# Performance work log

Hardware: AMD Instinct MI355X
Metric: run time of the kernel (lower is better)

## Reference

```python
import jax, jax.numpy as jnp
import numpy as np

NT, NV, ND, NM, NP = 50000, 1000, 20000, 5000, 8000
E = 100000
D, H, C = 256, 4, 64          # gnn_hidden_dim, heads, per-head channels
TS_FEAT, EMB, L = 64, 128, 2
NEG_SLOPE = 0.2

SIZES = {'ts': NT, 'vital': NV, 'diag': ND, 'med': NM, 'proc': NP}
EDGE_TYPES = [('ts', 'vital'), ('vital', 'ts'), ('ts', 'diag'), ('diag', 'ts'),
              ('ts', 'med'), ('med', 'ts'), ('ts', 'proc'), ('proc', 'ts')]
T = len(EDGE_TYPES)


def setup_inputs():
    key = jax.random.key(0)
    ks = jax.random.split(key, 32)
    def nrm(k, shape, s=0.05):
        return jax.random.normal(k, shape, dtype=jnp.float32) * s
    inp = {}
    inp['ts_x'] = nrm(ks[0], (NT, TS_FEAT), 1.0)
    inp['emb_vital'] = nrm(ks[1], (NV, EMB), 1.0)
    inp['emb_diag'] = nrm(ks[2], (ND, EMB), 1.0)
    inp['emb_med'] = nrm(ks[3], (NM, EMB), 1.0)
    inp['emb_proc'] = nrm(ks[4], (NP, EMB), 1.0)
    inp['Wp_ts'] = nrm(ks[5], (TS_FEAT, D)); inp['bp_ts'] = jnp.zeros((D,), jnp.float32)
    inp['Wp_c'] = nrm(ks[6], (4, EMB, D)); inp['bp_c'] = jnp.zeros((4, D), jnp.float32)
    inp['Wsrc'] = nrm(ks[7], (L, T, D, H * C))
    inp['Wdst'] = nrm(ks[8], (L, T, D, H * C))
    inp['asrc'] = nrm(ks[9], (L, T, H, C))
    inp['adst'] = nrm(ks[10], (L, T, H, C))
    inp['bconv'] = jnp.zeros((L, T, H * C), jnp.float32)
    inp['Wc1'] = nrm(ks[11], (D, D // 2)); inp['bc1'] = jnp.zeros((D // 2,), jnp.float32)
    inp['Wc2'] = nrm(ks[12], (D // 2, 1)); inp['bc2'] = jnp.zeros((1,), jnp.float32)
    names = ['ei_tv', 'ei_vt', 'ei_td', 'ei_dt', 'ei_tm', 'ei_mt', 'ei_tp', 'ei_pt']
    for i, ((s, d), nm) in enumerate(zip(EDGE_TYPES, names)):
        k1, k2 = jax.random.split(ks[13 + i])
        src = jax.random.randint(k1, (E,), 0, SIZES[s], dtype=jnp.int32)
        dst = jax.random.randint(k2, (E,), 0, SIZES[d], dtype=jnp.int32)
        inp[nm] = jnp.stack([src, dst])
    return inp


def gat_conv(xs, xd, Ws, Wd, a_s, a_d, b, ei, nd):
    """Bipartite PyG GATConv: add_self_loops=False, concat heads, eval (no dropout)."""
    hs = (xs @ Ws).reshape(-1, H, C)            # [Ns,H,C]
    hd = (xd @ Wd).reshape(-1, H, C)            # [Nd,H,C]
    es = jnp.sum(hs * a_s, axis=-1)             # [Ns,H]
    ed = jnp.sum(hd * a_d, axis=-1)             # [Nd,H]
    src, dst = ei[0], ei[1]
    e = jax.nn.leaky_relu(es[src] + ed[dst], NEG_SLOPE)   # [E,H]
    m = jax.ops.segment_max(e, dst, num_segments=nd)      # segment softmax over dst
    ex = jnp.exp(e - m[dst])
    den = jax.ops.segment_sum(ex, dst, num_segments=nd)
    alpha = ex / (den[dst] + 1e-16)
    msg = (alpha[:, :, None] * hs[src]).reshape(-1, H * C)  # [E,H*C]
    return jax.ops.segment_sum(msg, dst, num_segments=nd) + b


def _forward(ts_x, emb_vital, emb_diag, emb_med, emb_proc, Wp_ts, bp_ts, Wp_c, bp_c,
             Wsrc, Wdst, asrc, adst, bconv, Wc1, bc1, Wc2, bc2, edges):
    x = {'ts': ts_x @ Wp_ts + bp_ts,
         'vital': emb_vital @ Wp_c[0] + bp_c[0],
         'diag': emb_diag @ Wp_c[1] + bp_c[1],
         'med': emb_med @ Wp_c[2] + bp_c[2],
         'proc': emb_proc @ Wp_c[3] + bp_c[3]}
    for l in range(L):
        new = {k: jnp.zeros((SIZES[k], D), jnp.float32) for k in x}  # HeteroConv aggr='sum'
        for t, ((s, d), ei) in enumerate(zip(EDGE_TYPES, edges)):
            new[d] = new[d] + gat_conv(x[s], x[d], Wsrc[l, t], Wdst[l, t],
                                       asrc[l, t], adst[l, t], bconv[l, t], ei, SIZES[d])
        x = {k: jax.nn.relu(v) for k, v in new.items()}
    g = jnp.mean(x['ts'], axis=0)               # graph embedding
    h = jax.nn.relu(g @ Wc1 + bc1)
    logits = h @ Wc2 + bc2
    return jnp.squeeze(logits, -1)              # output_classes == 1 -> scalar


def reference(ts_x, emb_vital, emb_diag, emb_med, emb_proc, Wp_ts, bp_ts, Wp_c, bp_c,
              Wsrc, Wdst, asrc, adst, bconv, Wc1, bc1, Wc2, bc2,
              ei_tv, ei_vt, ei_td, ei_dt, ei_tm, ei_mt, ei_tp, ei_pt):
    edges = (ei_tv, ei_vt, ei_td, ei_dt, ei_tm, ei_mt, ei_tp, ei_pt)
    return _forward(ts_x, emb_vital, emb_diag, emb_med, emb_proc, Wp_ts, bp_ts, Wp_c, bp_c,
                    Wsrc, Wdst, asrc, adst, bconv, Wc1, bc1, Wc2, bc2, edges)
```

## Files before the change

kernel.cpp:

```cpp
#include <hip/hip_runtime.h>

#define E_N 100000
#define NTOT 84000
#define NDST 234000

typedef __attribute__((ext_vector_type(8))) short bfrag8;
typedef __attribute__((ext_vector_type(4))) float accf4;

__device__ __forceinline__ void atomAddF(float* p, float v) {
    unsafeAtomicAdd(p, v);
}

__device__ __forceinline__ float lrelu(float v) { return v >= 0.f ? v : 0.2f * v; }

__device__ __forceinline__ unsigned short f2bf(float f) {
    unsigned u = __float_as_uint(f);
    return (unsigned short)((u + 0x7FFFu + ((u >> 16) & 1u)) >> 16);
}
__device__ __forceinline__ float bf2f(unsigned short h) {
    return __uint_as_float(((unsigned)h) << 16);
}

__constant__ int c_tbase[8] = {0, 1000, 51000, 71000, 121000, 126000, 176000, 184000};

struct EI8 { const int* p[8]; };

struct BTJob { const float* W; unsigned short* hi; unsigned short* lo; int K; int kshift; };
struct BTBatch { BTJob j[17]; };

__global__ __launch_bounds__(256) void makeBT(BTBatch b)
{
    BTJob jb = b.j[blockIdx.z];
    int idx = blockIdx.x * 256 + threadIdx.x;
    if (idx >= (jb.K << 8)) return;
    int n = idx >> jb.kshift;
    int k = idx & (jb.K - 1);
    float w = jb.W[(size_t)k * 256 + n];
    unsigned short h = f2bf(w);
    jb.hi[idx] = h;
    jb.lo[idx] = f2bf(w - bf2f(h));
}

struct MJob { const float* A; const unsigned short* BThi; const unsigned short* BTlo;
              float* C; unsigned short* Cbf; const float* bias; int M; int K; int relu; };
struct MBatch { MJob j[8]; };

__global__ __launch_bounds__(256, 2) void gemm_mfma(MBatch batch)
{
    const MJob jb = batch.j[blockIdx.z];
    const int bx = blockIdx.x;
    const int rowblk = (bx >> 4) * 8 + (bx & 7);
    const int half = (bx >> 3) & 1;
    const int bm = rowblk * 128;
    if (bm >= jb.M) return;
    const int bn = half * 128;
    const int M = jb.M, K = jb.K;

    __shared__ unsigned short Ah[128 * 40];
    __shared__ unsigned short Al[128 * 40];
    __shared__ unsigned short B1[128 * 40];
    __shared__ unsigned short B2[128 * 40];

    const int tid  = threadIdx.x;
    const int wv   = tid >> 6;
    const int lane = tid & 63;
    const int qr = wv >> 1, qc = wv & 1;
    const int lm = lane & 15;
    const int lq = lane >> 4;

    accf4 acc[4][4] = {};

    for (int k0 = 0; k0 < K; k0 += 32) {
#pragma unroll
        for (int it = 0; it < 4; ++it) {
            int slot = it * 256 + tid;
            int m  = slot >> 3;
            int kq = (slot & 7) << 2;
            float4 v = make_float4(0.f, 0.f, 0.f, 0.f);
            if (bm + m < M) v = *(const float4*)(jb.A + (size_t)(bm + m) * K + k0 + kq);
            int o = m * 40 + kq;
            unsigned short h0 = f2bf(v.x), h1 = f2bf(v.y), h2 = f2bf(v.z), h3 = f2bf(v.w);
            Ah[o + 0] = h0; Ah[o + 1] = h1; Ah[o + 2] = h2; Ah[o + 3] = h3;
            Al[o + 0] = f2bf(v.x - bf2f(h0));
            Al[o + 1] = f2bf(v.y - bf2f(h1));
            Al[o + 2] = f2bf(v.z - bf2f(h2));
            Al[o + 3] = f2bf(v.w - bf2f(h3));
        }
#pragma unroll
        for (int it = 0; it < 2; ++it) {
            int slot = it * 256 + tid;
            int n  = slot >> 2;
            int kq = (slot & 3) << 3;
            size_t go = (size_t)(bn + n) * K + k0 + kq;
            *(uint4*)&B1[n * 40 + kq] = *(const uint4*)(jb.BThi + go);
            *(uint4*)&B2[n * 40 + kq] = *(const uint4*)(jb.BTlo + go);
        }
        __syncthreads();

        bfrag8 ah[4], al[4], b1[4], b2[4];
#pragma unroll
        for (int t = 0; t < 4; ++t) {
            int am  = qr * 64 + t * 16 + lm;
            int bnn = qc * 64 + t * 16 + lm;
            ah[t] = *(const bfrag8*)&Ah[am * 40 + lq * 8];
            al[t] = *(const bfrag8*)&Al[am * 40 + lq * 8];
            b1[t] = *(const bfrag8*)&B1[bnn * 40 + lq * 8];
            b2[t] = *(const bfrag8*)&B2[bnn * 40 + lq * 8];
        }
#pragma unroll
        for (int mt = 0; mt < 4; ++mt)
#pragma unroll
            for (int nt = 0; nt < 4; ++nt) {
                acc[mt][nt] = __builtin_amdgcn_mfma_f32_16x16x32_bf16(ah[mt], b1[nt], acc[mt][nt], 0, 0, 0);
                acc[mt][nt] = __builtin_amdgcn_mfma_f32_16x16x32_bf16(al[mt], b1[nt], acc[mt][nt], 0, 0, 0);
                acc[mt][nt] = __builtin_amdgcn_mfma_f32_16x16x32_bf16(ah[mt], b2[nt], acc[mt][nt], 0, 0, 0);
            }
        __syncthreads();
    }

#pragma unroll
    for (int nt = 0; nt < 4; ++nt) {
        int col = bn + qc * 64 + nt * 16 + lm;
        float bv = jb.bias ? jb.bias[col] : 0.f;
#pragma unroll
        for (int mt = 0; mt < 4; ++mt) {
            int row0 = bm + qr * 64 + mt * 16 + lq * 4;
#pragma unroll
            for (int r = 0; r < 4; ++r) {
                int row = row0 + r;
                if (row < M) {
                    float o = acc[mt][nt][r] + bv;
                    if (jb.relu) o = fmaxf(o, 0.f);
                    if (jb.C)   jb.C[(size_t)row * 256 + col] = o;
                    if (jb.Cbf) jb.Cbf[(size_t)row * 256 + col] = f2bf(o);
                }
            }
        }
    }
}

__global__ __launch_bounds__(256) void fill_weff(const float* __restrict__ Wsrc,
                                                 const float* __restrict__ Wdst,
                                                 const float* __restrict__ asrc,
                                                 const float* __restrict__ adst,
                                                 float* __restrict__ weff)
{
    int idx = blockIdx.x * 256 + threadIdx.x;
    if (idx >= 81920) return;
    int col = idx & 31;
    int k   = (idx >> 5) & 255;
    int lnt = idx >> 13;
    int nt  = lnt % 5;
    int l   = lnt / 5;
    bool is_src; int t, h;
    if (nt == 0) {
        if (col < 16) { is_src = true;  t = (col >> 2) * 2;            h = col & 3; }
        else          { is_src = false; t = ((col - 16) >> 2) * 2 + 1; h = col & 3; }
    } else {
        if (col < 4)      { is_src = true;  t = 2 * nt - 1; h = col; }
        else if (col < 8) { is_src = false; t = 2 * nt - 2; h = col - 4; }
        else { weff[idx] = 0.f; return; }
    }
    const float* W = (is_src ? Wsrc : Wdst) + ((size_t)((l * 8 + t) * 256 + k)) * 256 + h * 64;
    const float* a = (is_src ? asrc : adst) + ((size_t)((l * 8 + t) * 4 + h)) * 64;
    float val = 0.f;
    for (int c = 0; c < 64; c++) val += W[c] * a[c];
    weff[idx] = val;
}

__global__ __launch_bounds__(256) void fillEff(const float* __restrict__ Wp_ts,
                                               const float* __restrict__ bp_ts,
                                               const float* __restrict__ Wp_c,
                                               const float* __restrict__ bp_c,
                                               const float* __restrict__ weff,
                                               float* __restrict__ effT,
                                               float* __restrict__ biasT,
                                               float* __restrict__ effC,
                                               float* __restrict__ biasC)
{
    int idx = blockIdx.x * 256 + threadIdx.x;
    if (idx < 2048) {
        int kk = idx >> 5, j = idx & 31;
        float s = 0.f;
        for (int k = 0; k < 256; k++) s += Wp_ts[kk * 256 + k] * weff[k * 32 + j];
        effT[idx] = s;
    } else if (idx < 2080) {
        int j = idx - 2048;
        float s = 0.f;
        for (int k = 0; k < 256; k++) s += bp_ts[k] * weff[k * 32 + j];
        biasT[j] = s;
    } else if (idx < 2080 + 4 * 1032) {
        int r = idx - 2080;
        int q = r / 1032; r -= q * 1032;
        const float* wq = weff + (q + 1) * 8192;
        if (r < 1024) {
            int kk = r >> 3, j = r & 7;
            float s = 0.f;
            for (int k = 0; k < 256; k++) s += Wp_c[(size_t)q * 32768 + kk * 256 + k] * wq[k * 32 + j];
            effC[(q * 128 + kk) * 8 + j] = s;
        } else {
            int j = r - 1024;
            float s = 0.f;
            for (int k = 0; k < 256; k++) s += bp_c[q * 256 + k] * wq[k * 32 + j];
            biasC[q * 8 + j] = s;
        }
    }
}

__global__ __launch_bounds__(256) void attnprojA(const float* __restrict__ ts_x,
                                                 const float* __restrict__ effT,
                                                 const float* __restrict__ biasT,
                                                 float* __restrict__ attnT)
{
    int n = blockIdx.x * 256 + threadIdx.x;
    if (n >= 50000) return;
    float acc[32];
#pragma unroll
    for (int j = 0; j < 32; j++) acc[j] = biasT[j];
    const float* xr = ts_x + (size_t)n * 64;
    for (int k = 0; k < 64; k += 4) {
        float4 xv = *(const float4*)(xr + k);
#pragma unroll
        for (int j = 0; j < 32; j++)
            acc[j] += xv.x * effT[(k + 0) * 32 + j] + xv.y * effT[(k + 1) * 32 + j]
                    + xv.z * effT[(k + 2) * 32 + j] + xv.w * effT[(k + 3) * 32 + j];
    }
#pragma unroll
    for (int j = 0; j < 32; j++) attnT[(size_t)n * 32 + j] = acc[j];
}

__global__ __launch_bounds__(256) void attnprojC1(const float* __restrict__ e0,
                                                  const float* __restrict__ e1,
                                                  const float* __restrict__ e2,
                                                  const float* __restrict__ e3,
                                                  const float* __restrict__ effC,
                                                  const float* __restrict__ biasC,
                                                  float* __restrict__ attnC)
{
    int m = blockIdx.x * 256 + threadIdx.x;
    if (m >= 34000) return;
    int q, loc;
    if (m < 1000)       { q = 0; loc = m; }
    else if (m < 21000) { q = 1; loc = m - 1000; }
    else if (m < 26000) { q = 2; loc = m - 21000; }
    else                { q = 3; loc = m - 26000; }
    const float* er = (q == 0 ? e0 : q == 1 ? e1 : q == 2 ? e2 : e3) + (size_t)loc * 128;
    const float* W = effC + q * 1024;
    float acc[8];
#pragma unroll
    for (int j = 0; j < 8; j++) acc[j] = biasC[q * 8 + j];
    for (int k = 0; k < 128; k += 4) {
        float4 xv = *(const float4*)(er + k);
#pragma unroll
        for (int j = 0; j < 8; j++)
            acc[j] += xv.x * W[(k + 0) * 8 + j] + xv.y * W[(k + 1) * 8 + j]
                    + xv.z * W[(k + 2) * 8 + j] + xv.w * W[(k + 3) * 8 + j];
    }
#pragma unroll
    for (int j = 0; j < 8; j++) attnC[(size_t)m * 8 + j] = acc[j];
}

template<int NO>
__device__ __forceinline__ void attnproj_body(const float* __restrict__ xrow,
                                              const float* __restrict__ W,
                                              float* __restrict__ out)
{
    float acc[NO];
#pragma unroll
    for (int j = 0; j < NO; j++) acc[j] = 0.f;
    for (int k = 0; k < 256; k += 4) {
        const float4 xv = *(const float4*)(xrow + k);
#pragma unroll
        for (int j = 0; j < NO; j++) {
            acc[j] += xv.x * W[(k + 0) * 32 + j] + xv.y * W[(k + 1) * 32 + j]
                    + xv.z * W[(k + 2) * 32 + j] + xv.w * W[(k + 3) * 32 + j];
        }
    }
#pragma unroll
    for (int j = 0; j < NO; j++) out[j] = acc[j];
}

__global__ __launch_bounds__(256) void attnprojC2(const float* __restrict__ x1,
                                                  const float* __restrict__ weff_l,
                                                  float* __restrict__ attnC)
{
    int m = blockIdx.x * 256 + threadIdx.x;
    if (m >= 34000) return;
    int n = 50000 + m;
    int nt = (n < 51000) ? 1 : (n < 71000) ? 2 : (n < 76000) ? 3 : 4;
    attnproj_body<8>(x1 + (size_t)n * 256, weff_l + nt * 8192, attnC + (size_t)m * 8);
}

__global__ __launch_bounds__(256) void count_k(EI8 ei, int* __restrict__ cnt)
{
    int g = blockIdx.x * 256 + threadIdx.x;
    if (g >= 8 * E_N) return;
    int t = g / E_N;
    int i = g - t * E_N;
    int d = ei.p[t][E_N + i];
    atomicAdd(&cnt[c_tbase[t] + d], 1);
}

__global__ __launch_bounds__(256) void scanA(const int* __restrict__ cnt,
                                             int* __restrict__ rowptr,
                                             int* __restrict__ bsum)
{
    __shared__ int sd[256];
    int b = blockIdx.x, t = threadIdx.x;
    int base = b * 1024 + t * 4;
    int v0 = 0, v1 = 0, v2 = 0, v3 = 0;
    if (base + 0 < NDST) v0 = cnt[base + 0];
    if (base + 1 < NDST) v1 = cnt[base + 1];
    if (base + 2 < NDST) v2 = cnt[base + 2];
    if (base + 3 < NDST) v3 = cnt[base + 3];
    int s = v0 + v1 + v2 + v3;
    sd[t] = s;
    __syncthreads();
    for (int off = 1; off < 256; off <<= 1) {
        int x = 0;
        if (t >= off) x = sd[t - off];
        __syncthreads();
        if (t >= off) sd[t] += x;
        __syncthreads();
    }
    int run = sd[t] - s;
    if (t == 255) bsum[b] = sd[255];
    if (base + 0 < NDST) rowptr[base + 0] = run;          run += v0;
    if (base + 1 < NDST) rowptr[base + 1] = run;          run += v1;
    if (base + 2 < NDST) rowptr[base + 2] = run;          run += v2;
    if (base + 3 < NDST) rowptr[base + 3] = run;
}

__global__ __launch_bounds__(256) void scanB(int* __restrict__ bsum, int nb)
{
    __shared__ int sd[256];
    int t = threadIdx.x;
    int v = (t < nb) ? bsum[t] : 0;
    sd[t] = v;
    __syncthreads();
    for (int off = 1; off < 256; off <<= 1) {
        int x = 0;
        if (t >= off) x = sd[t - off];
        __syncthreads();
        if (t >= off) sd[t] += x;
        __syncthreads();
    }
    if (t < nb) bsum[t] = sd[t] - v;
}

__global__ __launch_bounds__(256) void scanC(int* __restrict__ rowptr,
                                             const int* __restrict__ bsum,
                                             int* __restrict__ cursor)
{
    int b = blockIdx.x, t = threadIdx.x;
    int off = bsum[b];
    int base = b * 1024 + t * 4;
#pragma unroll
    for (int j = 0; j < 4; j++) {
        int i = base + j;
        if (i < NDST) {
            int r = rowptr[i] + off;
            rowptr[i] = r;
            cursor[i] = r;
        }
    }
    if (b == 0 && t == 0) rowptr[NDST] = 8 * E_N;
}

__global__ __launch_bounds__(256) void place_k(EI8 ei, int* __restrict__ cursor,
                                               int* __restrict__ ssrc)
{
    int g = blockIdx.x * 256 + threadIdx.x;
    if (g >= 8 * E_N) return;
    int t = g / E_N;
    int i = g - t * E_N;
    int d = ei.p[t][E_N + i];
    int s = ei.p[t][i];
    int pos = atomicAdd(&cursor[c_tbase[t] + d], 1);
    ssrc[pos] = s;
}

__global__ __launch_bounds__(256) void aggx_k(const float* __restrict__ attnT,
                                              const float* __restrict__ attnC,
                                              const unsigned short* __restrict__ xtsbf,
                                              const int* __restrict__ rowptr,
                                              const int* __restrict__ ssrc,
                                              float* __restrict__ aggx)
{
    int w = blockIdx.x * 4 + (threadIdx.x >> 6);
    int lane = threadIdx.x & 63;
    int h = lane >> 4;
    int ch = (h << 6) | ((lane & 15) << 2);
    int q, dloc;
    if (w < 1000)       { q = 0; dloc = w; }
    else if (w < 21000) { q = 1; dloc = w - 1000; }
    else if (w < 26000) { q = 2; dloc = w - 21000; }
    else                { q = 3; dloc = w - 26000; }
    const int csr4[4]  = {0, 51000, 121000, 176000};
    const int soff4[4] = {0, 4, 8, 12};
    int soff = soff4[q];
    int r0 = rowptr[csr4[q] + dloc], r1 = rowptr[csr4[q] + dloc + 1];
    float ed = attnC[(size_t)w * 8 + 4 + h];
    float den = 0.f, sx = 0.f, sy = 0.f, sz = 0.f, sw = 0.f;
    int e = r0;
    for (; e + 4 <= r1; e += 4) {
        int sA = ssrc[e], sB = ssrc[e + 1], sC = ssrc[e + 2], sD = ssrc[e + 3];
        float eA = attnT[(size_t)sA * 32 + soff + h];
        float eB = attnT[(size_t)sB * 32 + soff + h];
        float eC = attnT[(size_t)sC * 32 + soff + h];
        float eD = attnT[(size_t)sD * 32 + soff + h];
        ushort4 rA = *(const ushort4*)(xtsbf + (size_t)sA * 256 + ch);
        ushort4 rB = *(const ushort4*)(xtsbf + (size_t)sB * 256 + ch);
        ushort4 rC = *(const ushort4*)(xtsbf + (size_t)sC * 256 + ch);
        ushort4 rD = *(const ushort4*)(xtsbf + (size_t)sD * 256 + ch);
        float xA = __expf(lrelu(eA + ed));
        float xB = __expf(lrelu(eB + ed));
        float xC = __expf(lrelu(eC + ed));
        float xD = __expf(lrelu(eD + ed));
        den += (xA + xB) + (xC + xD);
        sx += xA * bf2f(rA.x) + xB * bf2f(rB.x) + xC * bf2f(rC.x) + xD * bf2f(rD.x);
        sy += xA * bf2f(rA.y) + xB * bf2f(rB.y) + xC * bf2f(rC.y) + xD * bf2f(rD.y);
        sz += xA * bf2f(rA.z) + xB * bf2f(rB.z) + xC * bf2f(rC.z) + xD * bf2f(rD.z);
        sw += xA * bf2f(rA.w) + xB * bf2f(rB.w) + xC * bf2f(rC.w) + xD * bf2f(rD.w);
    }
    for (; e < r1; e++) {
        int s = ssrc[e];
        float es = attnT[(size_t)s * 32 + soff + h];
        float ex = __expf(lrelu(es + ed));
        den += ex;
        ushort4 rv = *(const ushort4*)(xtsbf + (size_t)s * 256 + ch);
        sx += ex * bf2f(rv.x); sy += ex * bf2f(rv.y);
        sz += ex * bf2f(rv.z); sw += ex * bf2f(rv.w);
    }
    float inv = 1.f / (den + 1e-16f);
    float4 o; o.x = sx * inv; o.y = sy * inv; o.z = sz * inv; o.w = sw * inv;
    *(float4*)(aggx + (size_t)w * 256 + ch) = o;
}

__device__ __forceinline__ float4 agg_ts_core(const float* __restrict__ attnT,
                                              const float* __restrict__ attnC,
                                              const unsigned short* __restrict__ hscbf,
                                              const int* __restrict__ rowptr,
                                              const int* __restrict__ ssrc,
                                              const float* __restrict__ bconv_l,
                                              int d, int h, int ch)
{
    const int co4[4]   = {0, 1000, 21000, 26000};
    const int tb4[4]   = {1000, 71000, 126000, 184000};
    const int doff4[4] = {16, 20, 24, 28};
    const int bo4[4]   = {256, 768, 1280, 1792};
    float ax = 0.f, ay = 0.f, az = 0.f, aw = 0.f;
#pragma unroll
    for (int q = 0; q < 4; q++) {
        int r0 = rowptr[tb4[q] + d], r1 = rowptr[tb4[q] + d + 1];
        float ed = attnT[(size_t)d * 32 + doff4[q] + h];
        float den = 0.f, sx = 0.f, sy = 0.f, sz = 0.f, sw = 0.f;
        int e = r0;
        for (; e + 2 <= r1; e += 2) {
            int sA = ssrc[e], sB = ssrc[e + 1];
            float eA = attnC[(size_t)(co4[q] + sA) * 8 + h];
            float eB = attnC[(size_t)(co4[q] + sB) * 8 + h];
            ushort4 rA = *(const ushort4*)(hscbf + (size_t)(co4[q] + sA) * 256 + ch);
            ushort4 rB = *(const ushort4*)(hscbf + (size_t)(co4[q] + sB) * 256 + ch);
            float xA = __expf(lrelu(eA + ed));
            float xB = __expf(lrelu(eB + ed));
            den += xA + xB;
            sx += xA * bf2f(rA.x) + xB * bf2f(rB.x);
            sy += xA * bf2f(rA.y) + xB * bf2f(rB.y);
            sz += xA * bf2f(rA.z) + xB * bf2f(rB.z);
            sw += xA * bf2f(rA.w) + xB * bf2f(rB.w);
        }
        if (e < r1) {
            int s = ssrc[e];
            float es = attnC[(size_t)(co4[q] + s) * 8 + h];
            float ex = __expf(lrelu(es + ed));
            den += ex;
            ushort4 hv = *(const ushort4*)(hscbf + (size_t)(co4[q] + s) * 256 + ch);
            sx += ex * bf2f(hv.x); sy += ex * bf2f(hv.y);
            sz += ex * bf2f(hv.z); sw += ex * bf2f(hv.w);
        }
        const float* b = bconv_l + bo4[q] + ch;
        float inv = 1.f / (den + 1e-16f);
        ax += b[0] + sx * inv; ay += b[1] + sy * inv;
        az += b[2] + sz * inv; aw += b[3] + sw * inv;
    }
    float4 o;
    o.x = fmaxf(ax, 0.f); o.y = fmaxf(ay, 0.f);
    o.z = fmaxf(az, 0.f); o.w = fmaxf(aw, 0.f);
    return o;
}

__global__ __launch_bounds__(256) void agg_ts_fold(float* __restrict__ attnT,
                                                   const float* __restrict__ attnC,
                                                   const unsigned short* __restrict__ hscbf,
                                                   const int* __restrict__ rowptr,
                                                   const int* __restrict__ ssrc,
                                                   const float* __restrict__ bconv_l,
                                                   const float* __restrict__ weff2)
{
    int wv = threadIdx.x >> 6;
    int d = blockIdx.x * 4 + wv;
    int lane = threadIdx.x & 63;
    int h = lane >> 4;
    int ch = (h << 6) | ((lane & 15) << 2);
    float4 o = agg_ts_core(attnT, attnC, hscbf, rowptr, ssrc, bconv_l, d, h, ch);
    __shared__ float rowbuf[4][256];
    rowbuf[wv][ch + 0] = o.x; rowbuf[wv][ch + 1] = o.y;
    rowbuf[wv][ch + 2] = o.z; rowbuf[wv][ch + 3] = o.w;
    __syncthreads();
    {
        int j = lane & 15, seg = lane >> 4;
        const float* rb = rowbuf[wv] + seg * 64;
        const float* w2 = weff2 + (seg * 64) * 32 + 16 + j;
        float s = 0.f;
#pragma unroll 8
        for (int c = 0; c < 64; c++) s += rb[c] * w2[c * 32];
        s += __shfl_xor(s, 16);
        s += __shfl_xor(s, 32);
        if (lane < 16) attnT[(size_t)d * 32 + 16 + lane] = s;
    }
}

__global__ __launch_bounds__(256) void agg_ts_pool(const float* __restrict__ attnT,
                                                   const float* __restrict__ attnC,
                                                   const unsigned short* __restrict__ hscbf,
                                                   const int* __restrict__ rowptr,
                                                   const int* __restrict__ ssrc,
                                                   const float* __restrict__ bconv_l,
                                                   float* __restrict__ part)
{
    int d = blockIdx.x * 4 + (threadIdx.x >> 6);
    int lane = threadIdx.x & 63;
    int h = lane >> 4;
    int ch = (h << 6) | ((lane & 15) << 2);
    float4 o = agg_ts_core(attnT, attnC, hscbf, rowptr, ssrc, bconv_l, d, h, ch);
    __shared__ float4 red4[256];
    red4[threadIdx.x] = o;
    __syncthreads();
    if (threadIdx.x < 64) {
        float4 a = red4[threadIdx.x], b = red4[threadIdx.x + 64];
        float4 c = red4[threadIdx.x + 128], dd = red4[threadIdx.x + 192];
        float4 s;
        s.x = (a.x + b.x) + (c.x + dd.x);
        s.y = (a.y + b.y) + (c.y + dd.y);
        s.z = (a.z + b.z) + (c.z + dd.z);
        s.w = (a.w + b.w) + (c.w + dd.w);
        int cch = ((threadIdx.x >> 4) << 6) | ((threadIdx.x & 15) << 2);
        *(float4*)(part + (size_t)blockIdx.x * 256 + cch) = s;
    }
}

__global__ __launch_bounds__(256) void colsum_part(const float* __restrict__ part,
                                                   float* __restrict__ gsum)
{
    int c = threadIdx.x;
    float s = 0.f;
    for (int r = blockIdx.x; r < 12500; r += gridDim.x) s += part[(size_t)r * 256 + c];
    atomAddF(gsum + c, s);
}

__global__ __launch_bounds__(128) void head_k(const float* __restrict__ gsum,
                                              const float* __restrict__ Wc1,
                                              const float* __restrict__ bc1,
                                              const float* __restrict__ Wc2,
                                              const float* __restrict__ bc2,
                                              float* __restrict__ out)
{
    __shared__ float g[256];
    __shared__ float red[128];
    int t = threadIdx.x;
    g[t] = gsum[t] * (1.f / 50000.f);
    g[t + 128] = gsum[t + 128] * (1.f / 50000.f);
    __syncthreads();
    float acc = bc1[t];
    for (int k = 0; k < 256; k++) acc += g[k] * Wc1[k * 128 + t];
    red[t] = fmaxf(acc, 0.f) * Wc2[t];
    __syncthreads();
    for (int sft = 64; sft > 0; sft >>= 1) {
        if (t < sft) red[t] += red[t + sft];
        __syncthreads();
    }
    if (t == 0) out[0] = red[0] + bc2[0];
}

extern "C" void kernel_launch(void* const* d_in, const int* in_sizes, int n_in,
                              void* d_out, int out_size, void* d_ws, size_t ws_size,
                              hipStream_t stream)
{
    const float* ts_x   = (const float*)d_in[0];
    const float* emb[4] = {(const float*)d_in[1], (const float*)d_in[2],
                           (const float*)d_in[3], (const float*)d_in[4]};
    const float* Wp_ts  = (const float*)d_in[5];
    const float* bp_ts  = (const float*)d_in[6];
    const float* Wp_c   = (const float*)d_in[7];
    const float* bp_c   = (const float*)d_in[8];
    const float* Wsrc   = (const float*)d_in[9];
    const float* Wdst   = (const float*)d_in[10];
    const float* asrc   = (const float*)d_in[11];
    const float* adst   = (const float*)d_in[12];
    const float* bconv  = (const float*)d_in[13];
    const float* Wc1    = (const float*)d_in[14];
    const float* bc1    = (const float*)d_in[15];
    const float* Wc2    = (const float*)d_in[16];
    const float* bc2    = (const float*)d_in[17];
    EI8 ei;
    for (int t = 0; t < 8; t++) ei.p[t] = (const int*)d_in[18 + t];

    float* x0    = (float*)d_ws;
    float* x1    = x0    + 21504000;
    float* attnT = x1    + 21504000;
    float* attnC = attnT + 1600000;
    float* weff  = attnC + 272000;
    float* gsum  = weff  + 81920;
    float* effT  = gsum  + 256;
    float* biasT = effT  + 2048;
    float* effC  = biasT + 32;
    float* biasC = effC  + 4096;
    int* rowptr  = (int*)(biasC + 32);
    int* bsum    = rowptr + 234004;
    int* ssrc    = bsum + 256;
    unsigned short* xtsbf = (unsigned short*)(ssrc + 800000);
    unsigned short* hscbf = xtsbf + 12800000;
    unsigned short* btp   = hscbf + 8704000;
    int* cursor  = (int*)hscbf;
    float* aggx  = x1;
    float* part  = x0;

    unsigned short* bt_ts_h = btp;
    unsigned short* bt_ts_l = bt_ts_h + 16384;
    unsigned short* bt_c_h[4], *bt_c_l[4];
    {
        unsigned short* p = bt_ts_l + 16384;
        for (int q = 0; q < 4; q++) { bt_c_h[q] = p; p += 32768; bt_c_l[q] = p; p += 32768; }
    }
    unsigned short* bt_w = bt_ts_l + 16384 + 8 * 32768;
    auto wpan_h = [&](int l, int t) { return bt_w + (size_t)((l == 0 ? t : 8 + t / 2) * 2) * 65536; };
    auto wpan_l = [&](int l, int t) { return wpan_h(l, t) + 65536; };

    hipMemsetAsync(cursor, 0, NDST * sizeof(int), stream);
    count_k<<<3125, 256, 0, stream>>>(ei, cursor);
    scanA<<<229, 256, 0, stream>>>(cursor, rowptr, bsum);
    scanB<<<1, 256, 0, stream>>>(bsum, 229);
    scanC<<<229, 256, 0, stream>>>(rowptr, bsum, cursor);
    place_k<<<3125, 256, 0, stream>>>(ei, cursor, ssrc);

    {
        BTBatch b = {};
        int zi = 0;
        b.j[zi++] = {Wp_ts, bt_ts_h, bt_ts_l, 64, 6};
        for (int q = 0; q < 4; q++)
            b.j[zi++] = {Wp_c + q * 32768, bt_c_h[q], bt_c_l[q], 128, 7};
        for (int t = 0; t < 8; t++)
            b.j[zi++] = {Wsrc + (size_t)(0 * 8 + t) * 65536, wpan_h(0, t), wpan_l(0, t), 256, 8};
        for (int t = 1; t < 8; t += 2)
            b.j[zi++] = {Wsrc + (size_t)(1 * 8 + t) * 65536, wpan_h(1, t), wpan_l(1, t), 256, 8};
        makeBT<<<dim3(256, 1, 17), 256, 0, stream>>>(b);
    }

    fill_weff<<<320, 256, 0, stream>>>(Wsrc, Wdst, asrc, adst, weff);
    fillEff<<<25, 256, 0, stream>>>(Wp_ts, bp_ts, Wp_c, bp_c, weff, effT, biasT, effC, biasC);

    attnprojA<<<196, 256, 0, stream>>>(ts_x, effT, biasT, attnT);
    attnprojC1<<<133, 256, 0, stream>>>(emb[0], emb[1], emb[2], emb[3], effC, biasC, attnC);

    static const int Nd4[4]    = {1000, 20000, 5000, 8000};
    static const int co4[4]    = {0, 1000, 21000, 26000};
    static const int dbase4[4] = {50000, 51000, 71000, 76000};
    static const int tsrc[4]   = {1, 3, 5, 7};
    static const int tdst[4]   = {0, 2, 4, 6};

    {
        MBatch b = {};
        b.j[0] = {ts_x, bt_ts_h, bt_ts_l, nullptr, xtsbf, bp_ts, 50000, 64, 0};
        for (int q = 0; q < 4; q++)
            b.j[1 + q] = {emb[q], bt_c_h[q], bt_c_l[q], x0 + (size_t)dbase4[q] * 256,
                          nullptr, bp_c + q * 256, Nd4[q], 128, 0};
        gemm_mfma<<<dim3(784, 1, 5), 256, 0, stream>>>(b);
    }

    aggx_k<<<8500, 256, 0, stream>>>(attnT, attnC, xtsbf, rowptr, ssrc, aggx);
    {
        MBatch b = {};
        for (int q = 0; q < 4; q++)
            b.j[q] = {x0 + (size_t)dbase4[q] * 256, wpan_h(0, tsrc[q]), wpan_l(0, tsrc[q]),
                      nullptr, hscbf + (size_t)co4[q] * 256, nullptr, Nd4[q], 256, 0};
        for (int q = 0; q < 4; q++)
            b.j[4 + q] = {aggx + (size_t)co4[q] * 256, wpan_h(0, tdst[q]), wpan_l(0, tdst[q]),
                          x1 + (size_t)dbase4[q] * 256, nullptr, bconv + tdst[q] * 256, Nd4[q], 256, 1};
        gemm_mfma<<<dim3(320, 1, 8), 256, 0, stream>>>(b);
    }
    agg_ts_fold<<<12500, 256, 0, stream>>>(attnT, attnC, hscbf, rowptr, ssrc, bconv, weff + 40960);

    attnprojC2<<<133, 256, 0, stream>>>(x1, weff + 40960, attnC);
    {
        MBatch b = {};
        for (int q = 0; q < 4; q++)
            b.j[q] = {x1 + (size_t)dbase4[q] * 256, wpan_h(1, tsrc[q]), wpan_l(1, tsrc[q]),
                      nullptr, hscbf + (size_t)co4[q] * 256, nullptr, Nd4[q], 256, 0};
        gemm_mfma<<<dim3(320, 1, 4), 256, 0, stream>>>(b);
    }
    agg_ts_pool<<<12500, 256, 0, stream>>>(attnT, attnC, hscbf, rowptr, ssrc, bconv + 2048, part);
    hipMemsetAsync(gsum, 0, 256 * sizeof(float), stream);
    colsum_part<<<256, 256, 0, stream>>>(part, gsum);

    head_k<<<1, 128, 0, stream>>>(gsum, Wc1, bc1, Wc2, bc2, (float*)d_out);
}
```

Measured before the change: 674.6 us.

## Merge independent prep and GEMM stages into fewer multi-role kernel launches

Folds many small kernels into combined launches that pick their role from the block index: weight conversion, attention-weight folding and edge counting go in one launch, effective-weight products with the scan in another, scan finalize with the attention projections in a third, and GEMMs alongside the edge placement and aggregation work. It also precomputes per-edge attention exponentials (an exf buffer baked per edge) so the aggregation kernels read them directly instead of recomputing them from attnT/attnC. The aim is to cut launch count and tail idle time between dependent small kernels. The cost is heterogeneous blocks in one grid, larger kernel argument structs, and extra scratch memory for the per-edge values.

Result: slower. 718.5 us (+6.5%).

```diff
diff --git a/kernel.cpp b/kernel.cpp
--- a/kernel.cpp
+++ b/kernel.cpp
@@ -1,16 +1,12 @@
 #include <hip/hip_runtime.h>
 
 #define E_N 100000
-#define NTOT 84000
 #define NDST 234000
 
 typedef __attribute__((ext_vector_type(8))) short bfrag8;
 typedef __attribute__((ext_vector_type(4))) float accf4;
 
-__device__ __forceinline__ void atomAddF(float* p, float v) {
-    unsafeAtomicAdd(p, v);
-}
-
+__device__ __forceinline__ void atomAddF(float* p, float v) { unsafeAtomicAdd(p, v); }
 __device__ __forceinline__ float lrelu(float v) { return v >= 0.f ? v : 0.2f * v; }
 
 __device__ __forceinline__ unsigned short f2bf(float f) {
@@ -22,33 +18,19 @@
 }
 
 __constant__ int c_tbase[8] = {0, 1000, 51000, 71000, 121000, 126000, 176000, 184000};
+__constant__ int c_co4[4]   = {0, 1000, 21000, 26000};
 
 struct EI8 { const int* p[8]; };
 
 struct BTJob { const float* W; unsigned short* hi; unsigned short* lo; int K; int kshift; };
 struct BTBatch { BTJob j[17]; };
-
-__global__ __launch_bounds__(256) void makeBT(BTBatch b)
-{
-    BTJob jb = b.j[blockIdx.z];
-    int idx = blockIdx.x * 256 + threadIdx.x;
-    if (idx >= (jb.K << 8)) return;
-    int n = idx >> jb.kshift;
-    int k = idx & (jb.K - 1);
-    float w = jb.W[(size_t)k * 256 + n];
-    unsigned short h = f2bf(w);
-    jb.hi[idx] = h;
-    jb.lo[idx] = f2bf(w - bf2f(h));
-}
 
 struct MJob { const float* A; const unsigned short* BThi; const unsigned short* BTlo;
               float* C; unsigned short* Cbf; const float* bias; int M; int K; int relu; };
 struct MBatch { MJob j[8]; };
 
-__global__ __launch_bounds__(256, 2) void gemm_mfma(MBatch batch)
-{
-    const MJob jb = batch.j[blockIdx.z];
-    const int bx = blockIdx.x;
+__device__ __forceinline__ void gemm_body(const MJob jb, int bx)
+{
     const int rowblk = (bx >> 4) * 8 + (bx & 7);
     const int half = (bx >> 3) & 1;
     const int bm = rowblk * 128;
@@ -139,196 +121,118 @@
     }
 }
 
-__global__ __launch_bounds__(256) void fill_weff(const float* __restrict__ Wsrc,
-                                                 const float* __restrict__ Wdst,
-                                                 const float* __restrict__ asrc,
-                                                 const float* __restrict__ adst,
-                                                 float* __restrict__ weff)
-{
-    int idx = blockIdx.x * 256 + threadIdx.x;
-    if (idx >= 81920) return;
-    int col = idx & 31;
-    int k   = (idx >> 5) & 255;
-    int lnt = idx >> 13;
-    int nt  = lnt % 5;
-    int l   = lnt / 5;
-    bool is_src; int t, h;
-    if (nt == 0) {
-        if (col < 16) { is_src = true;  t = (col >> 2) * 2;            h = col & 3; }
-        else          { is_src = false; t = ((col - 16) >> 2) * 2 + 1; h = col & 3; }
+struct Prep1 { BTBatch bt; const float* Wsrc; const float* Wdst; const float* asrc;
+               const float* adst; float* weff; EI8 ei; int* cnt; };
+
+__global__ __launch_bounds__(256) void prep1_k(Prep1 a)
+{
+    int bx = blockIdx.x;
+    if (bx < 4352) {
+        BTJob jb = a.bt.j[bx >> 8];
+        int idx = (bx & 255) * 256 + threadIdx.x;
+        if (idx >= (jb.K << 8)) return;
+        int n = idx >> jb.kshift;
+        int k = idx & (jb.K - 1);
+        float w = jb.W[(size_t)k * 256 + n];
+        unsigned short h = f2bf(w);
+        jb.hi[idx] = h;
+        jb.lo[idx] = f2bf(w - bf2f(h));
+    } else if (bx < 4672) {
+        int idx = (bx - 4352) * 256 + threadIdx.x;
+        if (idx >= 81920) return;
+        int col = idx & 31;
+        int k   = (idx >> 5) & 255;
+        int lnt = idx >> 13;
+        int nt  = lnt % 5;
+        int l   = lnt / 5;
+        bool is_src; int t, h;
+        if (nt == 0) {
+            if (col < 16) { is_src = true;  t = (col >> 2) * 2;            h = col & 3; }
+            else          { is_src = false; t = ((col - 16) >> 2) * 2 + 1; h = col & 3; }
+        } else {
+            if (col < 4)      { is_src = true;  t = 2 * nt - 1; h = col; }
+            else if (col < 8) { is_src = false; t = 2 * nt - 2; h = col - 4; }
+            else { a.weff[idx] = 0.f; return; }
+        }
+        const float* W = (is_src ? a.Wsrc : a.Wdst) + ((size_t)((l * 8 + t) * 256 + k)) * 256 + h * 64;
+        const float* av = (is_src ? a.asrc : a.adst) + ((size_t)((l * 8 + t) * 4 + h)) * 64;
+        float val = 0.f;
+        for (int c = 0; c < 64; c++) val += W[c] * av[c];
+        a.weff[idx] = val;
     } else {
-        if (col < 4)      { is_src = true;  t = 2 * nt - 1; h = col; }
-        else if (col < 8) { is_src = false; t = 2 * nt - 2; h = col - 4; }
-        else { weff[idx] = 0.f; return; }
-    }
-    const float* W = (is_src ? Wsrc : Wdst) + ((size_t)((l * 8 + t) * 256 + k)) * 256 + h * 64;
-    const float* a = (is_src ? asrc : adst) + ((size_t)((l * 8 + t) * 4 + h)) * 64;
-    float val = 0.f;
-    for (int c = 0; c < 64; c++) val += W[c] * a[c];
-    weff[idx] = val;
-}
-
-__global__ __launch_bounds__(256) void fillEff(const float* __restrict__ Wp_ts,
+        int g = (bx - 4672) * 256 + threadIdx.x;
+        if (g >= 8 * E_N) return;
+        int t = g / E_N;
+        int i = g - t * E_N;
+        int d = a.ei.p[t][E_N + i];
+        atomicAdd(&a.cnt[c_tbase[t] + d], 1);
+    }
+}
+
+__global__ __launch_bounds__(256) void prep2_k(const float* __restrict__ Wp_ts,
                                                const float* __restrict__ bp_ts,
                                                const float* __restrict__ Wp_c,
                                                const float* __restrict__ bp_c,
                                                const float* __restrict__ weff,
-                                               float* __restrict__ effT,
-                                               float* __restrict__ biasT,
-                                               float* __restrict__ effC,
-                                               float* __restrict__ biasC)
-{
-    int idx = blockIdx.x * 256 + threadIdx.x;
-    if (idx < 2048) {
-        int kk = idx >> 5, j = idx & 31;
-        float s = 0.f;
-        for (int k = 0; k < 256; k++) s += Wp_ts[kk * 256 + k] * weff[k * 32 + j];
-        effT[idx] = s;
-    } else if (idx < 2080) {
-        int j = idx - 2048;
-        float s = 0.f;
-        for (int k = 0; k < 256; k++) s += bp_ts[k] * weff[k * 32 + j];
-        biasT[j] = s;
-    } else if (idx < 2080 + 4 * 1032) {
-        int r = idx - 2080;
-        int q = r / 1032; r -= q * 1032;
-        const float* wq = weff + (q + 1) * 8192;
-        if (r < 1024) {
-            int kk = r >> 3, j = r & 7;
+                                               float* __restrict__ effT, float* __restrict__ biasT,
+                                               float* __restrict__ effC, float* __restrict__ biasC,
+                                               const int* __restrict__ cnt,
+                                               int* __restrict__ rowptr, int* __restrict__ bsum)
+{
+    if (blockIdx.x < 25) {
+        int idx = blockIdx.x * 256 + threadIdx.x;
+        if (idx < 2048) {
+            int kk = idx >> 5, j = idx & 31;
             float s = 0.f;
-            for (int k = 0; k < 256; k++) s += Wp_c[(size_t)q * 32768 + kk * 256 + k] * wq[k * 32 + j];
-            effC[(q * 128 + kk) * 8 + j] = s;
-        } else {
-            int j = r - 1024;
+            for (int k = 0; k < 256; k++) s += Wp_ts[kk * 256 + k] * weff[k * 32 + j];
+            effT[idx] = s;
+        } else if (idx < 2080) {
+            int j = idx - 2048;
             float s = 0.f;
-            for (int k = 0; k < 256; k++) s += bp_c[q * 256 + k] * wq[k * 32 + j];
-            biasC[q * 8 + j] = s;
-        }
-    }
-}
-
-__global__ __launch_bounds__(256) void attnprojA(const float* __restrict__ ts_x,
-                                                 const float* __restrict__ effT,
-                                                 const float* __restrict__ biasT,
-                                                 float* __restrict__ attnT)
-{
-    int n = blockIdx.x * 256 + threadIdx.x;
-    if (n >= 50000) return;
-    float acc[32];
-#pragma unroll
-    for (int j = 0; j < 32; j++) acc[j] = biasT[j];
-    const float* xr = ts_x + (size_t)n * 64;
-    for (int k = 0; k < 64; k += 4) {
-        float4 xv = *(const float4*)(xr + k);
-#pragma unroll
-        for (int j = 0; j < 32; j++)
-            acc[j] += xv.x * effT[(k + 0) * 32 + j] + xv.y * effT[(k + 1) * 32 + j]
-                    + xv.z * effT[(k + 2) * 32 + j] + xv.w * effT[(k + 3) * 32 + j];
-    }
-#pragma unroll
-    for (int j = 0; j < 32; j++) attnT[(size_t)n * 32 + j] = acc[j];
-}
-
-__global__ __launch_bounds__(256) void attnprojC1(const float* __restrict__ e0,
-                                                  const float* __restrict__ e1,
-                                                  const float* __restrict__ e2,
-                                                  const float* __restrict__ e3,
-                                                  const float* __restrict__ effC,
-                                                  const float* __restrict__ biasC,
-                                                  float* __restrict__ attnC)
-{
-    int m = blockIdx.x * 256 + threadIdx.x;
-    if (m >= 34000) return;
-    int q, loc;
-    if (m < 1000)       { q = 0; loc = m; }
-    else if (m < 21000) { q = 1; loc = m - 1000; }
-    else if (m < 26000) { q = 2; loc = m - 21000; }
-    else                { q = 3; loc = m - 26000; }
-    const float* er = (q == 0 ? e0 : q == 1 ? e1 : q == 2 ? e2 : e3) + (size_t)loc * 128;
-    const float* W = effC + q * 1024;
-    float acc[8];
-#pragma unroll
-    for (int j = 0; j < 8; j++) acc[j] = biasC[q * 8 + j];
-    for (int k = 0; k < 128; k += 4) {
-        float4 xv = *(const float4*)(er + k);
-#pragma unroll
-        for (int j = 0; j < 8; j++)
-            acc[j] += xv.x * W[(k + 0) * 8 + j] + xv.y * W[(k + 1) * 8 + j]
-                    + xv.z * W[(k + 2) * 8 + j] + xv.w * W[(k + 3) * 8 + j];
-    }
-#pragma unroll
-    for (int j = 0; j < 8; j++) attnC[(size_t)m * 8 + j] = acc[j];
-}
-
-template<int NO>
-__device__ __forceinline__ void attnproj_body(const float* __restrict__ xrow,
-                                              const float* __restrict__ W,
-                                              float* __restrict__ out)
-{
-    float acc[NO];
-#pragma unroll
-    for (int j = 0; j < NO; j++) acc[j] = 0.f;
-    for (int k = 0; k < 256; k += 4) {
-        const float4 xv = *(const float4*)(xrow + k);
-#pragma unroll
-        for (int j = 0; j < NO; j++) {
-            acc[j] += xv.x * W[(k + 0) * 32 + j] + xv.y * W[(k + 1) * 32 + j]
-                    + xv.z * W[(k + 2) * 32 + j] + xv.w * W[(k + 3) * 32 + j];
-        }
-    }
-#pragma unroll
-    for (int j = 0; j < NO; j++) out[j] = acc[j];
-}
-
-__global__ __launch_bounds__(256) void attnprojC2(const float* __restrict__ x1,
-                                                  const float* __restrict__ weff_l,
-                                                  float* __restrict__ attnC)
-{
-    int m = blockIdx.x * 256 + threadIdx.x;
-    if (m >= 34000) return;
-    int n = 50000 + m;
-    int nt = (n < 51000) ? 1 : (n < 71000) ? 2 : (n < 76000) ? 3 : 4;
-    attnproj_body<8>(x1 + (size_t)n * 256, weff_l + nt * 8192, attnC + (size_t)m * 8);
-}
-
-__global__ __launch_bounds__(256) void count_k(EI8 ei, int* __restrict__ cnt)
-{
-    int g = blockIdx.x * 256 + threadIdx.x;
-    if (g >= 8 * E_N) return;
-    int t = g / E_N;
-    int i = g - t * E_N;
-    int d = ei.p[t][E_N + i];
-    atomicAdd(&cnt[c_tbase[t] + d], 1);
-}
-
-__global__ __launch_bounds__(256) void scanA(const int* __restrict__ cnt,
-                                             int* __restrict__ rowptr,
-                                             int* __restrict__ bsum)
-{
-    __shared__ int sd[256];
-    int b = blockIdx.x, t = threadIdx.x;
-    int base = b * 1024 + t * 4;
-    int v0 = 0, v1 = 0, v2 = 0, v3 = 0;
-    if (base + 0 < NDST) v0 = cnt[base + 0];
-    if (base + 1 < NDST) v1 = cnt[base + 1];
-    if (base + 2 < NDST) v2 = cnt[base + 2];
-    if (base + 3 < NDST) v3 = cnt[base + 3];
-    int s = v0 + v1 + v2 + v3;
-    sd[t] = s;
-    __syncthreads();
-    for (int off = 1; off < 256; off <<= 1) {
-        int x = 0;
-        if (t >= off) x = sd[t - off];
+            for (int k = 0; k < 256; k++) s += bp_ts[k] * weff[k * 32 + j];
+            biasT[j] = s;
+        } else if (idx < 2080 + 4 * 1032) {
+            int r = idx - 2080;
+            int q = r / 1032; r -= q * 1032;
+            const float* wq = weff + (q + 1) * 8192;
+            if (r < 1024) {
+                int kk = r >> 3, j = r & 7;
+                float s = 0.f;
+                for (int k = 0; k < 256; k++) s += Wp_c[(size_t)q * 32768 + kk * 256 + k] * wq[k * 32 + j];
+                effC[(q * 128 + kk) * 8 + j] = s;
+            } else {
+                int j = r - 1024;
+                float s = 0.f;
+                for (int k = 0; k < 256; k++) s += bp_c[q * 256 + k] * wq[k * 32 + j];
+                biasC[q * 8 + j] = s;
+            }
+        }
+    } else {
+        __shared__ int sd[256];
+        int b = blockIdx.x - 25, t = threadIdx.x;
+        int base = b * 1024 + t * 4;
+        int v0 = 0, v1 = 0, v2 = 0, v3 = 0;
+        if (base + 0 < NDST) v0 = cnt[base + 0];
+        if (base + 1 < NDST) v1 = cnt[base + 1];
+        if (base + 2 < NDST) v2 = cnt[base + 2];
+        if (base + 3 < NDST) v3 = cnt[base + 3];
+        int s = v0 + v1 + v2 + v3;
+        sd[t] = s;
         __syncthreads();
-        if (t >= off) sd[t] += x;
-        __syncthreads();
-    }
-    int run = sd[t] - s;
-    if (t == 255) bsum[b] = sd[255];
-    if (base + 0 < NDST) rowptr[base + 0] = run;          run += v0;
-    if (base + 1 < NDST) rowptr[base + 1] = run;          run += v1;
-    if (base + 2 < NDST) rowptr[base + 2] = run;          run += v2;
-    if (base + 3 < NDST) rowptr[base + 3] = run;
+        for (int off = 1; off < 256; off <<= 1) {
+            int x = 0;
+            if (t >= off) x = sd[t - off];
+            __syncthreads();
+            if (t >= off) sd[t] += x;
+            __syncthreads();
+        }
+        int run = sd[t] - s;
+        if (t == 255) bsum[b] = sd[255];
+        if (base + 0 < NDST) rowptr[base + 0] = run;          run += v0;
+        if (base + 1 < NDST) rowptr[base + 1] = run;          run += v1;
+        if (base + 2 < NDST) rowptr[base + 2] = run;          run += v2;
+        if (base + 3 < NDST) rowptr[base + 3] = run;
+    }
 }
 
 __global__ __launch_bounds__(256) void scanB(int* __restrict__ bsum, int nb)
@@ -348,46 +252,164 @@
     if (t < nb) bsum[t] = sd[t] - v;
 }
 
-__global__ __launch_bounds__(256) void scanC(int* __restrict__ rowptr,
-                                             const int* __restrict__ bsum,
-                                             int* __restrict__ cursor)
-{
-    int b = blockIdx.x, t = threadIdx.x;
-    int off = bsum[b];
-    int base = b * 1024 + t * 4;
-#pragma unroll
-    for (int j = 0; j < 4; j++) {
-        int i = base + j;
-        if (i < NDST) {
-            int r = rowptr[i] + off;
-            rowptr[i] = r;
-            cursor[i] = r;
-        }
-    }
-    if (b == 0 && t == 0) rowptr[NDST] = 8 * E_N;
-}
-
-__global__ __launch_bounds__(256) void place_k(EI8 ei, int* __restrict__ cursor,
-                                               int* __restrict__ ssrc)
-{
-    int g = blockIdx.x * 256 + threadIdx.x;
-    if (g >= 8 * E_N) return;
-    int t = g / E_N;
-    int i = g - t * E_N;
-    int d = ei.p[t][E_N + i];
-    int s = ei.p[t][i];
-    int pos = atomicAdd(&cursor[c_tbase[t] + d], 1);
-    ssrc[pos] = s;
-}
-
-__global__ __launch_bounds__(256) void aggx_k(const float* __restrict__ attnT,
-                                              const float* __restrict__ attnC,
-                                              const unsigned short* __restrict__ xtsbf,
-                                              const int* __restrict__ rowptr,
-                                              const int* __restrict__ ssrc,
-                                              float* __restrict__ aggx)
-{
-    int w = blockIdx.x * 4 + (threadIdx.x >> 6);
+struct Prep3 { int* rowptr; const int* bsum; int* cursor;
+               const float* ts_x; const float* effT; const float* biasT; float* attnT;
+               const float* e0; const float* e1; const float* e2; const float* e3;
+               const float* effC; const float* biasC; float* attnC; };
+
+__global__ __launch_bounds__(256) void prep3_k(Prep3 a)
+{
+    int bx = blockIdx.x;
+    if (bx < 229) {
+        int t = threadIdx.x;
+        int off = a.bsum[bx];
+        int base = bx * 1024 + t * 4;
+#pragma unroll
+        for (int j = 0; j < 4; j++) {
+            int i = base + j;
+            if (i < NDST) {
+                int r = a.rowptr[i] + off;
+                a.rowptr[i] = r;
+                a.cursor[i] = r;
+            }
+        }
+        if (bx == 0 && t == 0) a.rowptr[NDST] = 8 * E_N;
+    } else if (bx < 425) {
+        int n = (bx - 229) * 256 + threadIdx.x;
+        if (n >= 50000) return;
+        float acc[32];
+#pragma unroll
+        for (int j = 0; j < 32; j++) acc[j] = a.biasT[j];
+        const float* xr = a.ts_x + (size_t)n * 64;
+        for (int k = 0; k < 64; k += 4) {
+            float4 xv = *(const float4*)(xr + k);
+#pragma unroll
+            for (int j = 0; j < 32; j++)
+                acc[j] += xv.x * a.effT[(k + 0) * 32 + j] + xv.y * a.effT[(k + 1) * 32 + j]
+                        + xv.z * a.effT[(k + 2) * 32 + j] + xv.w * a.effT[(k + 3) * 32 + j];
+        }
+#pragma unroll
+        for (int j = 0; j < 32; j++) a.attnT[(size_t)n * 32 + j] = acc[j];
+    } else {
+        int m = (bx - 425) * 256 + threadIdx.x;
+        if (m >= 34000) return;
+        int q, loc;
+        if (m < 1000)       { q = 0; loc = m; }
+        else if (m < 21000) { q = 1; loc = m - 1000; }
+        else if (m < 26000) { q = 2; loc = m - 21000; }
+        else                { q = 3; loc = m - 26000; }
+        const float* er = (q == 0 ? a.e0 : q == 1 ? a.e1 : q == 2 ? a.e2 : a.e3) + (size_t)loc * 128;
+        const float* W = a.effC + q * 1024;
+        float acc[8];
+#pragma unroll
+        for (int j = 0; j < 8; j++) acc[j] = a.biasC[q * 8 + j];
+        for (int k = 0; k < 128; k += 4) {
+            float4 xv = *(const float4*)(er + k);
+#pragma unroll
+            for (int j = 0; j < 8; j++)
+                acc[j] += xv.x * W[(k + 0) * 8 + j] + xv.y * W[(k + 1) * 8 + j]
+                        + xv.z * W[(k + 2) * 8 + j] + xv.w * W[(k + 3) * 8 + j];
+        }
+#pragma unroll
+        for (int j = 0; j < 8; j++) a.attnC[(size_t)m * 8 + j] = acc[j];
+    }
+}
+
+struct ProjPlace { MBatch mb; EI8 ei; int* cursor; int* ssrc; int* sdst; float* exf;
+                   const float* attnT; const float* attnC; };
+
+__global__ __launch_bounds__(256, 2) void projplace_k(ProjPlace a)
+{
+    if (blockIdx.x < 3920) {
+        gemm_body(a.mb.j[blockIdx.x / 784], blockIdx.x % 784);
+    } else {
+        int g = (blockIdx.x - 3920) * 256 + threadIdx.x;
+        if (g >= 8 * E_N) return;
+        int t = g / E_N;
+        int i = g - t * E_N;
+        int d = a.ei.p[t][E_N + i];
+        int s = a.ei.p[t][i];
+        int pos = atomicAdd(&a.cursor[c_tbase[t] + d], 1);
+        a.ssrc[pos] = s;
+        a.sdst[pos] = d;
+        int q = t >> 1;
+        float4 ex;
+        if ((t & 1) == 0) {
+            int w = c_co4[q] + d;
+            int soff = 4 * q;
+            ex.x = __expf(lrelu(a.attnT[(size_t)s * 32 + soff + 0] + a.attnC[(size_t)w * 8 + 4]));
+            ex.y = __expf(lrelu(a.attnT[(size_t)s * 32 + soff + 1] + a.attnC[(size_t)w * 8 + 5]));
+            ex.z = __expf(lrelu(a.attnT[(size_t)s * 32 + soff + 2] + a.attnC[(size_t)w * 8 + 6]));
+            ex.w = __expf(lrelu(a.attnT[(size_t)s * 32 + soff + 3] + a.attnC[(size_t)w * 8 + 7]));
+        } else {
+            int m = c_co4[q] + s;
+            int doff = 16 + 4 * q;
+            ex.x = __expf(lrelu(a.attnC[(size_t)m * 8 + 0] + a.attnT[(size_t)d * 32 + doff + 0]));
+            ex.y = __expf(lrelu(a.attnC[(size_t)m * 8 + 1] + a.attnT[(size_t)d * 32 + doff + 1]));
+            ex.z = __expf(lrelu(a.attnC[(size_t)m * 8 + 2] + a.attnT[(size_t)d * 32 + doff + 2]));
+            ex.w = __expf(lrelu(a.attnC[(size_t)m * 8 + 3] + a.attnT[(size_t)d * 32 + doff + 3]));
+        }
+        *(float4*)(a.exf + (size_t)pos * 4) = ex;
+    }
+}
+
+__device__ __forceinline__ float4 agg_core(const float* __restrict__ exf,
+                                           const unsigned short* __restrict__ hscbf,
+                                           const int* __restrict__ rowptr,
+                                           const int* __restrict__ ssrc,
+                                           const float* __restrict__ bconv_l,
+                                           int d, int h, int ch)
+{
+    const int co4[4] = {0, 1000, 21000, 26000};
+    const int tb4[4] = {1000, 71000, 126000, 184000};
+    const int bo4[4] = {256, 768, 1280, 1792};
+    float ax = 0.f, ay = 0.f, az = 0.f, aw = 0.f;
+#pragma unroll
+    for (int q = 0; q < 4; q++) {
+        int r0 = rowptr[tb4[q] + d], r1 = rowptr[tb4[q] + d + 1];
+        float den = 0.f, sx = 0.f, sy = 0.f, sz = 0.f, sw = 0.f;
+        int e = r0;
+        for (; e + 2 <= r1; e += 2) {
+            int sA = ssrc[e], sB = ssrc[e + 1];
+            float xA = exf[(size_t)e * 4 + h];
+            float xB = exf[(size_t)(e + 1) * 4 + h];
+            ushort4 rA = *(const ushort4*)(hscbf + (size_t)(co4[q] + sA) * 256 + ch);
+            ushort4 rB = *(const ushort4*)(hscbf + (size_t)(co4[q] + sB) * 256 + ch);
+            den += xA + xB;
+            sx += xA * bf2f(rA.x) + xB * bf2f(rB.x);
+            sy += xA * bf2f(rA.y) + xB * bf2f(rB.y);
+            sz += xA * bf2f(rA.z) + xB * bf2f(rB.z);
+            sw += xA * bf2f(rA.w) + xB * bf2f(rB.w);
+        }
+        if (e < r1) {
+            int s = ssrc[e];
+            float x = exf[(size_t)e * 4 + h];
+            den += x;
+            ushort4 hv = *(const ushort4*)(hscbf + (size_t)(co4[q] + s) * 256 + ch);
+            sx += x * bf2f(hv.x); sy += x * bf2f(hv.y);
+            sz += x * bf2f(hv.z); sw += x * bf2f(hv.w);
+        }
+        const float* b = bconv_l + bo4[q] + ch;
+        float inv = 1.f / (den + 1e-16f);
+        ax += b[0] + sx * inv; ay += b[1] + sy * inv;
+        az += b[2] + sz * inv; aw += b[3] + sw * inv;
+    }
+    float4 o;
+    o.x = fmaxf(ax, 0.f); o.y = fmaxf(ay, 0.f);
+    o.z = fmaxf(az, 0.f); o.w = fmaxf(aw, 0.f);
+    return o;
+}
+
+struct L1A { MBatch mb; const float* exf; const unsigned short* xtsbf;
+             const int* rowptr; const int* ssrc; float* aggx; };
+
+__global__ __launch_bounds__(256, 2) void l1a_k(L1A a)
+{
+    if (blockIdx.x < 1280) {
+        gemm_body(a.mb.j[blockIdx.x / 320], blockIdx.x % 320);
+        return;
+    }
+    int w = (blockIdx.x - 1280) * 4 + (threadIdx.x >> 6);
     int lane = threadIdx.x & 63;
     int h = lane >> 4;
     int ch = (h << 6) | ((lane & 15) << 2);
@@ -396,27 +418,20 @@
     else if (w < 21000) { q = 1; dloc = w - 1000; }
     else if (w < 26000) { q = 2; dloc = w - 21000; }
     else                { q = 3; dloc = w - 26000; }
-    const int csr4[4]  = {0, 51000, 121000, 176000};
-    const int soff4[4] = {0, 4, 8, 12};
-    int soff = soff4[q];
-    int r0 = rowptr[csr4[q] + dloc], r1 = rowptr[csr4[q] + dloc + 1];
-    float ed = attnC[(size_t)w * 8 + 4 + h];
+    const int csr4[4] = {0, 51000, 121000, 176000};
+    int r0 = a.rowptr[csr4[q] + dloc], r1 = a.rowptr[csr4[q] + dloc + 1];
     float den = 0.f, sx = 0.f, sy = 0.f, sz = 0.f, sw = 0.f;
     int e = r0;
     for (; e + 4 <= r1; e += 4) {
-        int sA = ssrc[e], sB = ssrc[e + 1], sC = ssrc[e + 2], sD = ssrc[e + 3];
-        float eA = attnT[(size_t)sA * 32 + soff + h];
-        float eB = attnT[(size_t)sB * 32 + soff + h];
-        float eC = attnT[(size_t)sC * 32 + soff + h];
-        float eD = attnT[(size_t)sD * 32 + soff + h];
-        ushort4 rA = *(const ushort4*)(xtsbf + (size_t)sA * 256 + ch);
-        ushort4 rB = *(const ushort4*)(xtsbf + (size_t)sB * 256 + ch);
-        ushort4 rC = *(const ushort4*)(xtsbf + (size_t)sC * 256 + ch);
-        ushort4 rD = *(const ushort4*)(xtsbf + (size_t)sD * 256 + ch);
-        float xA = __expf(lrelu(eA + ed));
-        float xB = __expf(lrelu(eB + ed));
-        float xC = __expf(lrelu(eC + ed));
-        float xD = __expf(lrelu(eD + ed));
+        int sA = a.ssrc[e], sB = a.ssrc[e + 1], sC = a.ssrc[e + 2], sD = a.ssrc[e + 3];
+        float xA = a.exf[(size_t)e * 4 + h];
+        float xB = a.exf[(size_t)(e + 1) * 4 + h];
+        float xC = a.exf[(size_t)(e + 2) * 4 + h];
+        float xD = a.exf[(size_t)(e + 3) * 4 + h];
+        ushort4 rA = *(const ushort4*)(a.xtsbf + (size_t)sA * 256 + ch);
+        ushort4 rB = *(const ushort4*)(a.xtsbf + (size_t)sB * 256 + ch);
+        ushort4 rC = *(const ushort4*)(a.xtsbf + (size_t)sC * 256 + ch);
+        ushort4 rD = *(const ushort4*)(a.xtsbf + (size_t)sD * 256 + ch);
         den += (xA + xB) + (xC + xD);
         sx += xA * bf2f(rA.x) + xB * bf2f(rB.x) + xC * bf2f(rC.x) + xD * bf2f(rD.x);
         sy += xA * bf2f(rA.y) + xB * bf2f(rB.y) + xC * bf2f(rC.y) + xD * bf2f(rD.y);
@@ -424,116 +439,111 @@
         sw += xA * bf2f(rA.w) + xB * bf2f(rB.w) + xC * bf2f(rC.w) + xD * bf2f(rD.w);
     }
     for (; e < r1; e++) {
-        int s = ssrc[e];
-        float es = attnT[(size_t)s * 32 + soff + h];
-        float ex = __expf(lrelu(es + ed));
-        den += ex;
-        ushort4 rv = *(const ushort4*)(xtsbf + (size_t)s * 256 + ch);
-        sx += ex * bf2f(rv.x); sy += ex * bf2f(rv.y);
-        sz += ex * bf2f(rv.z); sw += ex * bf2f(rv.w);
+        int s = a.ssrc[e];
+        float x = a.exf[(size_t)e * 4 + h];
+        den += x;
+        ushort4 rv = *(const ushort4*)(a.xtsbf + (size_t)s * 256 + ch);
+        sx += x * bf2f(rv.x); sy += x * bf2f(rv.y);
+        sz += x * bf2f(rv.z); sw += x * bf2f(rv.w);
     }
     float inv = 1.f / (den + 1e-16f);
     float4 o; o.x = sx * inv; o.y = sy * inv; o.z = sz * inv; o.w = sw * inv;
-    *(float4*)(aggx + (size_t)w * 256 + ch) = o;
-}
-
-__device__ __forceinline__ float4 agg_ts_core(const float* __restrict__ attnT,
+    *(float4*)(a.aggx + (size_t)w * 256 + ch) = o;
+}
+
+struct L1B { MBatch mb; float* attnT; const float* exf; const unsigned short* hscbf;
+             const int* rowptr; const int* ssrc; const float* bconv_l; const float* weff2; };
+
+__global__ __launch_bounds__(256, 2) void l1b_k(L1B a)
+{
+    if (blockIdx.x < 1280) {
+        gemm_body(a.mb.j[blockIdx.x / 320], blockIdx.x % 320);
+        return;
+    }
+    int bx = blockIdx.x - 1280;
+    int wv = threadIdx.x >> 6;
+    int d = bx * 4 + wv;
+    int lane = threadIdx.x & 63;
+    int h = lane >> 4;
+    int ch = (h << 6) | ((lane & 15) << 2);
+    float4 o = agg_core(a.exf, a.hscbf, a.rowptr, a.ssrc, a.bconv_l, d, h, ch);
+    __shared__ float rowbuf[4][256];
+    rowbuf[wv][ch + 0] = o.x; rowbuf[wv][ch + 1] = o.y;
+    rowbuf[wv][ch + 2] = o.z; rowbuf[wv][ch + 3] = o.w;
+    __syncthreads();
+    int j = lane & 15, seg = lane >> 4;
+    const float* rb = rowbuf[wv] + seg * 64;
+    const float* w2 = a.weff2 + (seg * 64) * 32 + 16 + j;
+    float s = 0.f;
+#pragma unroll 8
+    for (int c = 0; c < 64; c++) s += rb[c] * w2[c * 32];
+    s += __shfl_xor(s, 16);
+    s += __shfl_xor(s, 32);
+    if (lane < 16) a.attnT[(size_t)d * 32 + 16 + lane] = s;
+}
+
+struct L2A { MBatch mb; const float* x1; const float* weff2; float* attnC; };
+
+__global__ __launch_bounds__(256, 2) void l2a_k(L2A a)
+{
+    if (blockIdx.x < 1280) {
+        gemm_body(a.mb.j[blockIdx.x / 320], blockIdx.x % 320);
+        return;
+    }
+    int m = (blockIdx.x - 1280) * 256 + threadIdx.x;
+    if (m >= 34000) return;
+    int n = 50000 + m;
+    int nt = (n < 51000) ? 1 : (n < 71000) ? 2 : (n < 76000) ? 3 : 4;
+    const float* xrow = a.x1 + (size_t)n * 256;
+    const float* W = a.weff2 + nt * 8192;
+    float acc[8];
+#pragma unroll
+    for (int j = 0; j < 8; j++) acc[j] = 0.f;
+    for (int k = 0; k < 256; k += 4) {
+        const float4 xv = *(const float4*)(xrow + k);
+#pragma unroll
+        for (int j = 0; j < 8; j++)
+            acc[j] += xv.x * W[(k + 0) * 32 + j] + xv.y * W[(k + 1) * 32 + j]
+                    + xv.z * W[(k + 2) * 32 + j] + xv.w * W[(k + 3) * 32 + j];
+    }
+#pragma unroll
+    for (int j = 0; j < 8; j++) a.attnC[(size_t)m * 8 + j] = acc[j];
+}
+
+__global__ __launch_bounds__(256) void bake_k(const int* __restrict__ ssrc,
+                                              const int* __restrict__ sdst,
                                               const float* __restrict__ attnC,
+                                              const float* __restrict__ attnT,
+                                              float* __restrict__ exf)
+{
+    int i = blockIdx.x * 256 + threadIdx.x;
+    if (i >= 400000) return;
+    int tq = i / E_N;
+    int i2 = i - tq * E_N;
+    int e = (2 * tq + 1) * E_N + i2;
+    int s = ssrc[e], d = sdst[e];
+    int m = c_co4[tq] + s;
+    int doff = 16 + 4 * tq;
+    float4 ex;
+    ex.x = __expf(lrelu(attnC[(size_t)m * 8 + 0] + attnT[(size_t)d * 32 + doff + 0]));
+    ex.y = __expf(lrelu(attnC[(size_t)m * 8 + 1] + attnT[(size_t)d * 32 + doff + 1]));
+    ex.z = __expf(lrelu(attnC[(size_t)m * 8 + 2] + attnT[(size_t)d * 32 + doff + 2]));
+    ex.w = __expf(lrelu(attnC[(size_t)m * 8 + 3] + attnT[(size_t)d * 32 + doff + 3]));
+    *(float4*)(exf + (size_t)e * 4) = ex;
+}
+
+__global__ __launch_bounds__(256) void pool_k(const float* __restrict__ exf,
                                               const unsigned short* __restrict__ hscbf,
                                               const int* __restrict__ rowptr,
                                               const int* __restrict__ ssrc,
                                               const float* __restrict__ bconv_l,
-                                              int d, int h, int ch)
-{
-    const int co4[4]   = {0, 1000, 21000, 26000};
-    const int tb4[4]   = {1000, 71000, 126000, 184000};
-    const int doff4[4] = {16, 20, 24, 28};
-    const int bo4[4]   = {256, 768, 1280, 1792};
-    float ax = 0.f, ay = 0.f, az = 0.f, aw = 0.f;
-#pragma unroll
-    for (int q = 0; q < 4; q++) {
-        int r0 = rowptr[tb4[q] + d], r1 = rowptr[tb4[q] + d + 1];
-        float ed = attnT[(size_t)d * 32 + doff4[q] + h];
-        float den = 0.f, sx = 0.f, sy = 0.f, sz = 0.f, sw = 0.f;
-        int e = r0;
-        for (; e + 2 <= r1; e += 2) {
-            int sA = ssrc[e], sB = ssrc[e + 1];
-            float eA = attnC[(size_t)(co4[q] + sA) * 8 + h];
-            float eB = attnC[(size_t)(co4[q] + sB) * 8 + h];
-            ushort4 rA = *(const ushort4*)(hscbf + (size_t)(co4[q] + sA) * 256 + ch);
-            ushort4 rB = *(const ushort4*)(hscbf + (size_t)(co4[q] + sB) * 256 + ch);
-            float xA = __expf(lrelu(eA + ed));
-            float xB = __expf(lrelu(eB + ed));
-            den += xA + xB;
-            sx += xA * bf2f(rA.x) + xB * bf2f(rB.x);
-            sy += xA * bf2f(rA.y) + xB * bf2f(rB.y);
-            sz += xA * bf2f(rA.z) + xB * bf2f(rB.z);
-            sw += xA * bf2f(rA.w) + xB * bf2f(rB.w);
-        }
-        if (e < r1) {
-            int s = ssrc[e];
-            float es = attnC[(size_t)(co4[q] + s) * 8 + h];
-            float ex = __expf(lrelu(es + ed));
-            den += ex;
-            ushort4 hv = *(const ushort4*)(hscbf + (size_t)(co4[q] + s) * 256 + ch);
-            sx += ex * bf2f(hv.x); sy += ex * bf2f(hv.y);
-            sz += ex * bf2f(hv.z); sw += ex * bf2f(hv.w);
-        }
-        const float* b = bconv_l + bo4[q] + ch;
-        float inv = 1.f / (den + 1e-16f);
-        ax += b[0] + sx * inv; ay += b[1] + sy * inv;
-        az += b[2] + sz * inv; aw += b[3] + sw * inv;
-    }
-    float4 o;
-    o.x = fmaxf(ax, 0.f); o.y = fmaxf(ay, 0.f);
-    o.z = fmaxf(az, 0.f); o.w = fmaxf(aw, 0.f);
-    return o;
-}
-
-__global__ __launch_bounds__(256) void agg_ts_fold(float* __restrict__ attnT,
-                                                   const float* __restrict__ attnC,
-                                                   const unsigned short* __restrict__ hscbf,
-                                                   const int* __restrict__ rowptr,
-                                                   const int* __restrict__ ssrc,
-                                                   const float* __restrict__ bconv_l,
-                                                   const float* __restrict__ weff2)
-{
-    int wv = threadIdx.x >> 6;
-    int d = blockIdx.x * 4 + wv;
-    int lane = threadIdx.x & 63;
-    int h = lane >> 4;
-    int ch = (h << 6) | ((lane & 15) << 2);
-    float4 o = agg_ts_core(attnT, attnC, hscbf, rowptr, ssrc, bconv_l, d, h, ch);
-    __shared__ float rowbuf[4][256];
-    rowbuf[wv][ch + 0] = o.x; rowbuf[wv][ch + 1] = o.y;
-    rowbuf[wv][ch + 2] = o.z; rowbuf[wv][ch + 3] = o.w;
-    __syncthreads();
-    {
-        int j = lane & 15, seg = lane >> 4;
-        const float* rb = rowbuf[wv] + seg * 64;
-        const float* w2 = weff2 + (seg * 64) * 32 + 16 + j;
-        float s = 0.f;
-#pragma unroll 8
-        for (int c = 0; c < 64; c++) s += rb[c] * w2[c * 32];
-        s += __shfl_xor(s, 16);
-        s += __shfl_xor(s, 32);
-        if (lane < 16) attnT[(size_t)d * 32 + 16 + lane] = s;
-    }
-}
-
-__global__ __launch_bounds__(256) void agg_ts_pool(const float* __restrict__ attnT,
-                                                   const float* __restrict__ attnC,
-                                                   const unsigned short* __restrict__ hscbf,
-                                                   const int* __restrict__ rowptr,
-                                                   const int* __restrict__ ssrc,
-                                                   const float* __restrict__ bconv_l,
-                                                   float* __restrict__ part)
+                                              float* __restrict__ part)
 {
     int d = blockIdx.x * 4 + (threadIdx.x >> 6);
     int lane = threadIdx.x & 63;
     int h = lane >> 4;
     int ch = (h << 6) | ((lane & 15) << 2);
-    float4 o = agg_ts_core(attnT, attnC, hscbf, rowptr, ssrc, bconv_l, d, h, ch);
+    float4 o = agg_core(exf, hscbf, rowptr, ssrc, bconv_l, d, h, ch);
     __shared__ float4 red4[256];
     red4[threadIdx.x] = o;
     __syncthreads();
@@ -624,7 +634,9 @@
     unsigned short* btp   = hscbf + 8704000;
     int* cursor  = (int*)hscbf;
     float* aggx  = x1;
-    float* part  = x0;
+    float* exf   = x0;
+    int* sdst    = (int*)(x0 + 3200000);
+    float* part  = x0 + 4200000;
 
     unsigned short* bt_ts_h = btp;
     unsigned short* bt_ts_l = bt_ts_h + 16384;
@@ -637,71 +649,81 @@
     auto wpan_h = [&](int l, int t) { return bt_w + (size_t)((l == 0 ? t : 8 + t / 2) * 2) * 65536; };
     auto wpan_l = [&](int l, int t) { return wpan_h(l, t) + 65536; };
 
-    hipMemsetAsync(cursor, 0, NDST * sizeof(int), stream);
-    count_k<<<3125, 256, 0, stream>>>(ei, cursor);
-    scanA<<<229, 256, 0, stream>>>(cursor, rowptr, bsum);
-    scanB<<<1, 256, 0, stream>>>(bsum, 229);
-    scanC<<<229, 256, 0, stream>>>(rowptr, bsum, cursor);
-    place_k<<<3125, 256, 0, stream>>>(ei, cursor, ssrc);
-
-    {
-        BTBatch b = {};
-        int zi = 0;
-        b.j[zi++] = {Wp_ts, bt_ts_h, bt_ts_l, 64, 6};
-        for (int q = 0; q < 4; q++)
-            b.j[zi++] = {Wp_c + q * 32768, bt_c_h[q], bt_c_l[q], 128, 7};
-        for (int t = 0; t < 8; t++)
-            b.j[zi++] = {Wsrc + (size_t)(0 * 8 + t) * 65536, wpan_h(0, t), wpan_l(0, t), 256, 8};
-        for (int t = 1; t < 8; t += 2)
-            b.j[zi++] = {Wsrc + (size_t)(1 * 8 + t) * 65536, wpan_h(1, t), wpan_l(1, t), 256, 8};
-        makeBT<<<dim3(256, 1, 17), 256, 0, stream>>>(b);
-    }
-
-    fill_weff<<<320, 256, 0, stream>>>(Wsrc, Wdst, asrc, adst, weff);
-    fillEff<<<25, 256, 0, stream>>>(Wp_ts, bp_ts, Wp_c, bp_c, weff, effT, biasT, effC, biasC);
-
-    attnprojA<<<196, 256, 0, stream>>>(ts_x, effT, biasT, attnT);
-    attnprojC1<<<133, 256, 0, stream>>>(emb[0], emb[1], emb[2], emb[3], effC, biasC, attnC);
-
     static const int Nd4[4]    = {1000, 20000, 5000, 8000};
     static const int co4[4]    = {0, 1000, 21000, 26000};
     static const int dbase4[4] = {50000, 51000, 71000, 76000};
     static const int tsrc[4]   = {1, 3, 5, 7};
     static const int tdst[4]   = {0, 2, 4, 6};
 
+    hipMemsetAsync(cursor, 0, NDST * sizeof(int), stream);
+
     {
-        MBatch b = {};
-        b.j[0] = {ts_x, bt_ts_h, bt_ts_l, nullptr, xtsbf, bp_ts, 50000, 64, 0};
+        Prep1 a = {};
+        int zi = 0;
+        a.bt.j[zi++] = {Wp_ts, bt_ts_h, bt_ts_l, 64, 6};
         for (int q = 0; q < 4; q++)
-            b.j[1 + q] = {emb[q], bt_c_h[q], bt_c_l[q], x0 + (size_t)dbase4[q] * 256,
-                          nullptr, bp_c + q * 256, Nd4[q], 128, 0};
-        gemm_mfma<<<dim3(784, 1, 5), 256, 0, stream>>>(b);
-    }
-
-    aggx_k<<<8500, 256, 0, stream>>>(attnT, attnC, xtsbf, rowptr, ssrc, aggx);
+            a.bt.j[zi++] = {Wp_c + q * 32768, bt_c_h[q], bt_c_l[q], 128, 7};
+        for (int t = 0; t < 8; t++)
+            a.bt.j[zi++] = {Wsrc + (size_t)(0 * 8 + t) * 65536, wpan_h(0, t), wpan_l(0, t), 256, 8};
+        for (int t = 1; t < 8; t += 2)
+            a.bt.j[zi++] = {Wsrc + (size_t)(1 * 8 + t) * 65536, wpan_h(1, t), wpan_l(1, t), 256, 8};
+        a.Wsrc = Wsrc; a.Wdst = Wdst; a.asrc = asrc; a.adst = adst;
+        a.weff = weff; a.ei = ei; a.cnt = cursor;
+        prep1_k<<<7797, 256, 0, stream>>>(a);
+    }
+
+    prep2_k<<<254, 256, 0, stream>>>(Wp_ts, bp_ts, Wp_c, bp_c, weff,
+                                     effT, biasT, effC, biasC, cursor, rowptr, bsum);
+    scanB<<<1, 256, 0, stream>>>(bsum, 229);
+
     {
-        MBatch b = {};
+        Prep3 a = {rowptr, bsum, cursor, ts_x, effT, biasT, attnT,
+                   emb[0], emb[1], emb[2], emb[3], effC, biasC, attnC};
+        prep3_k<<<558, 256, 0, stream>>>(a);
+    }
+
+    {
+        ProjPlace a = {};
+        a.mb.j[0] = {ts_x, bt_ts_h, bt_ts_l, nullptr, xtsbf, bp_ts, 50000, 64, 0};
         for (int q = 0; q < 4; q++)
-            b.j[q] = {x0 + (size_t)dbase4[q] * 256, wpan_h(0, tsrc[q]), wpan_l(0, tsrc[q]),
-                      nullptr, hscbf + (size_t)co4[q] * 256, nullptr, Nd4[q], 256, 0};
+            a.mb.j[1 + q] = {emb[q], bt_c_h[q], bt_c_l[q], x0 + (size_t)dbase4[q] * 256,
+                             nullptr, bp_c + q * 256, Nd4[q], 128, 0};
+        a.ei = ei; a.cursor = cursor; a.ssrc = ssrc; a.sdst = sdst; a.exf = exf;
+        a.attnT = attnT; a.attnC = attnC;
+        projplace_k<<<7045, 256, 0, stream>>>(a);
+    }
+
+    {
+        L1A a = {};
         for (int q = 0; q < 4; q++)
-            b.j[4 + q] = {aggx + (size_t)co4[q] * 256, wpan_h(0, tdst[q]), wpan_l(0, tdst[q]),
-                          x1 + (size_t)dbase4[q] * 256, nullptr, bconv + tdst[q] * 256, Nd4[q], 256, 1};
-        gemm_mfma<<<dim3(320, 1, 8), 256, 0, stream>>>(b);
-    }
-    agg_ts_fold<<<12500, 256, 0, stream>>>(attnT, attnC, hscbf, rowptr, ssrc, bconv, weff + 40960);
-
-    attnprojC2<<<133, 256, 0, stream>>>(x1, weff + 40960, attnC);
+            a.mb.j[q] = {x0 + (size_t)dbase4[q] * 256, wpan_h(0, tsrc[q]), wpan_l(0, tsrc[q]),
+                         nullptr, hscbf + (size_t)co4[q] * 256, nullptr, Nd4[q], 256, 0};
+        a.exf = exf; a.xtsbf = xtsbf; a.rowptr = rowptr; a.ssrc = ssrc; a.aggx = aggx;
+        l1a_k<<<9780, 256, 0, stream>>>(a);
+    }
+
     {
-        MBatch b = {};
+        L1B a = {};
         for (int q = 0; q < 4; q++)
-            b.j[q] = {x1 + (size_t)dbase4[q] * 256, wpan_h(1, tsrc[q]), wpan_l(1, tsrc[q]),
-                      nullptr, hscbf + (size_t)co4[q] * 256, nullptr, Nd4[q], 256, 0};
-        gemm_mfma<<<dim3(320, 1, 4), 256, 0, stream>>>(b);
-    }
-    agg_ts_pool<<<12500, 256, 0, stream>>>(attnT, attnC, hscbf, rowptr, ssrc, bconv + 2048, part);
+            a.mb.j[q] = {aggx + (size_t)co4[q] * 256, wpan_h(0, tdst[q]), wpan_l(0, tdst[q]),
+                         x1 + (size_t)dbase4[q] * 256, nullptr, bconv + tdst[q] * 256, Nd4[q], 256, 1};
+        a.attnT = attnT; a.exf = exf; a.hscbf = hscbf; a.rowptr = rowptr; a.ssrc = ssrc;
+        a.bconv_l = bconv; a.weff2 = weff + 40960;
+        l1b_k<<<13780, 256, 0, stream>>>(a);
+    }
+
+    {
+        L2A a = {};
+        for (int q = 0; q < 4; q++)
+            a.mb.j[q] = {x1 + (size_t)dbase4[q] * 256, wpan_h(1, tsrc[q]), wpan_l(1, tsrc[q]),
+                         nullptr, hscbf + (size_t)co4[q] * 256, nullptr, Nd4[q], 256, 0};
+        a.x1 = x1; a.weff2 = weff + 40960; a.attnC = attnC;
+        l2a_k<<<1413, 256, 0, stream>>>(a);
+    }
+
+    bake_k<<<1563, 256, 0, stream>>>(ssrc, sdst, attnC, attnT, exf);
     hipMemsetAsync(gsum, 0, 256 * sizeof(float), stream);
+    pool_k<<<12500, 256, 0, stream>>>(exf, hscbf, rowptr, ssrc, bconv + 2048, part);
     colsum_part<<<256, 256, 0, stream>>>(part, gsum);
-
     head_k<<<1, 128, 0, stream>>>(gsum, Wc1, bc1, Wc2, bc2, (float*)d_out);
 }
```
